# Optimization experiments

Measured on AMD Instinct MI355X. Metric: run time of the kernel, lower is better.

## Reference

```python
import jax, jax.numpy as jnp
import numpy as np

K = 3
TOP_K = 10
MASK_RATIO = 0.5
EPS_COS = 1e-8
EPS_DEG = 1e-6


def setup_inputs() -> dict:
    key = jax.random.key(0)
    ks = jax.random.split(key, 10)
    N, C, H, O, E = 4096, 128, 128, 64, 65536
    x = jax.random.normal(ks[0], (N, C), dtype=jnp.float32)
    edge_index = jax.random.randint(ks[1], (2, E), 0, N, dtype=jnp.int64)
    alpha = jnp.full((K,), 1.0 / K, dtype=jnp.float32)
    fusion_W = 0.02 * jax.random.normal(ks[2], (2 * H, H), dtype=jnp.float32)
    fusion_b = jnp.zeros((H,), dtype=jnp.float32)
    lin0_W = 0.02 * jax.random.normal(ks[3], (C, H), dtype=jnp.float32)
    lin0_b = jnp.zeros((H,), dtype=jnp.float32)
    lin1_W = 0.02 * jax.random.normal(ks[4], (H, O), dtype=jnp.float32)
    lin1_b = jnp.zeros((O,), dtype=jnp.float32)
    return {
        "x": x, "edge_index": edge_index, "alpha": alpha,
        "fusion_W": fusion_W, "fusion_b": fusion_b,
        "lin0_W": lin0_W, "lin0_b": lin0_b,
        "lin1_W": lin1_W, "lin1_b": lin1_b,
    }


def reference(x, edge_index, alpha, fusion_W, fusion_b, lin0_W, lin0_b, lin1_W, lin1_b):
    N = x.shape[0]
    # dense adjacency and its powers: A^0 = I (so A^0 @ x = x), A^1, A^2
    A = jnp.zeros((N, N), x.dtype).at[edge_index[0], edge_index[1]].set(1.0)
    A2 = A @ A
    hop_feats = jnp.stack([x, A @ x, A2 @ x], axis=0)  # [K, N, C]

    # per-node cosine-similarity top-k (self always included, cos=1)
    xn = x / (jnp.linalg.norm(x, axis=-1, keepdims=True) + EPS_COS)
    sim = xn @ xn.T  # [N, N]
    _, topk_idx = jax.lax.top_k(sim, TOP_K)  # [N, TOP_K]

    # random keep-mask per node, forced True at top-k neighbors
    mask = jax.random.uniform(jax.random.key(42), (N, N)) < MASK_RATIO
    rows = jnp.arange(N)[:, None]
    mask = mask.at[rows, topk_idx].set(True)
    Mf = mask.astype(x.dtype)  # [N, N]

    # alpha-weighted multi-hop aggregate, masked mean over selected nodes
    agg = jnp.einsum('k,knc->nc', alpha, hop_feats)  # [N, C]
    fused = (Mf @ agg) / (Mf.sum(axis=1, keepdims=True) + EPS_DEG)  # [N, C]

    h = jnp.concatenate([x, fused], axis=-1) @ fusion_W + fusion_b
    h = jax.nn.relu(h @ lin0_W + lin0_b)  # dropout inactive in eval
    out = h @ lin1_W + lin1_b
    return jax.nn.log_softmax(out, axis=1)
```

## Files before the change

### kernel.cpp

```cpp
#include <hip/hip_runtime.h>
#include <hip/hip_bf16.h>
#include <stdint.h>


#define N_NODES 4096
#define C_DIM   128
#define WPR     128
#define HALF_P  8388608u
#define TOPK    10
#define LSTR    13
#define JSPLIT  4

typedef __attribute__((ext_vector_type(8))) short bf16x8;
typedef __attribute__((ext_vector_type(4))) float f32x4;

__device__ __forceinline__ uint16_t f2bf(float f) {
    uint32_t u = __float_as_uint(f);
    return (uint16_t)((u + 0x7FFFu + ((u >> 16) & 1u)) >> 16);
}

__device__ __forceinline__ uint32_t rotl32(uint32_t v, int r) {
    return (v << r) | (v >> (32 - r));
}

__device__ __forceinline__ void threefry2x32(uint32_t k0, uint32_t k1,
                                             uint32_t x0, uint32_t x1,
                                             uint32_t& o0, uint32_t& o1) {
    uint32_t ks2 = k0 ^ k1 ^ 0x1BD11BDAu;
    x0 += k0; x1 += k1;
#define TF_ROUND(r) { x0 += x1; x1 = rotl32(x1, (r)); x1 ^= x0; }
    TF_ROUND(13) TF_ROUND(15) TF_ROUND(26) TF_ROUND(6)
    x0 += k1;  x1 += ks2 + 1u;
    TF_ROUND(17) TF_ROUND(29) TF_ROUND(16) TF_ROUND(24)
    x0 += ks2; x1 += k0 + 2u;
    TF_ROUND(13) TF_ROUND(15) TF_ROUND(26) TF_ROUND(6)
    x0 += k0;  x1 += k1 + 3u;
    TF_ROUND(17) TF_ROUND(29) TF_ROUND(16) TF_ROUND(24)
    x0 += k1;  x1 += ks2 + 4u;
    TF_ROUND(13) TF_ROUND(15) TF_ROUND(26) TF_ROUND(6)
    x0 += ks2; x1 += k0 + 5u;
#undef TF_ROUND
    o0 = x0; o1 = x1;
}

__global__ void scatter_kernel(const int* __restrict__ ei, int E,
                               uint32_t* __restrict__ Abits) {
    __shared__ int cnt_oddnz;
    int t = threadIdx.x;
    if (t == 0) cnt_oddnz = 0;
    __syncthreads();
    if (((const uint32_t*)ei)[2 * t + 1] != 0u) atomicAdd(&cnt_oddnz, 1);
    __syncthreads();
    bool is64 = (cnt_oddnz <= 8);
    int e = blockIdx.x * blockDim.x + t;
    if (e >= E) return;
    int src, dst;
    if (is64) { src = ei[2 * e]; dst = ei[2 * (E + e)]; }
    else      { src = ei[e];     dst = ei[E + e]; }
    src &= (N_NODES - 1);
    dst &= (N_NODES - 1);
    atomicOr(&Abits[src * WPR + (dst >> 5)], 1u << (dst & 31));
}

__global__ void spmm_kernel(const uint32_t* __restrict__ Abits,
                            const float* __restrict__ in,
                            float* __restrict__ out) {
    int i = blockIdx.x;
    int c = threadIdx.x;
    __shared__ uint32_t wbits[WPR];
    wbits[c] = Abits[i * WPR + c];
    __syncthreads();
    float acc = 0.f;
    for (int w = 0; w < WPR; ++w) {
        uint32_t bits = wbits[w];
        while (bits) {
            int b = __ffs(bits) - 1;
            bits &= bits - 1;
            acc += in[(w * 32 + b) * C_DIM + c];
        }
    }
    out[i * C_DIM + c] = acc;
}

__global__ void spmm2_agg_kernel(const uint32_t* __restrict__ Abits,
                                 const float* __restrict__ hop1,
                                 const float* __restrict__ xf,
                                 const float* __restrict__ alpha,
                                 float* __restrict__ agg) {
    int i = blockIdx.x;
    int c = threadIdx.x;
    __shared__ uint32_t wbits[WPR];
    wbits[c] = Abits[i * WPR + c];
    __syncthreads();
    float acc = 0.f;
    for (int w = 0; w < WPR; ++w) {
        uint32_t bits = wbits[w];
        while (bits) {
            int b = __ffs(bits) - 1;
            bits &= bits - 1;
            acc += hop1[(w * 32 + b) * C_DIM + c];
        }
    }
    agg[i * C_DIM + c] = alpha[0] * xf[i * C_DIM + c]
                       + alpha[1] * hop1[i * C_DIM + c]
                       + alpha[2] * acc;
}

__global__ void norm_kernel(const float* __restrict__ xf,
                            uint16_t* __restrict__ xnb) {
    int i = blockIdx.x;
    int c = threadIdx.x;
    float v = xf[i * C_DIM + c];
    float sq = v * v;
    #pragma unroll
    for (int off = 32; off >= 1; off >>= 1) sq += __shfl_xor(sq, off);
    __shared__ float ws[2];
    if ((c & 63) == 0) ws[c >> 6] = sq;
    __syncthreads();
    float tot = ws[0] + ws[1];
    xnb[i * C_DIM + c] = f2bf(v / (sqrtf(tot) + 1e-8f));
}

__global__ void transpose_bf_kernel(const float* __restrict__ agg,
                                    uint16_t* __restrict__ aggTb) {
    __shared__ float tile[32][33];
    int bi = blockIdx.x;
    int bc = blockIdx.y;
    int tx = threadIdx.x & 31, ty = threadIdx.x >> 5;
    #pragma unroll
    for (int r = 0; r < 32; r += 8)
        tile[ty + r][tx] = agg[(size_t)(bi * 32 + ty + r) * C_DIM + bc * 32 + tx];
    __syncthreads();
    #pragma unroll
    for (int r = 0; r < 32; r += 8)
        aggTb[(size_t)(bc * 32 + ty + r) * N_NODES + bi * 32 + tx] =
            f2bf(tile[tx][ty + r]);
}

__global__ void mask_kernel(uint32_t* __restrict__ Mbits,
                            int* __restrict__ degpre) {
    uint32_t tid = blockIdx.x * blockDim.x + threadIdx.x;
    uint32_t base = tid * 32u;
    uint32_t w0 = 0u, w1 = 0u;
    for (int k = 0; k < 32; ++k) {
        uint32_t o0, o1;
        threefry2x32(0u, 42u, base + k, HALF_P + base + k, o0, o1);
        w0 |= (uint32_t)((o0 >> 31) ^ 1u) << k;
        w1 |= (uint32_t)((o1 >> 31) ^ 1u) << k;
    }
    Mbits[tid] = w0;
    Mbits[(HALF_P >> 5) + tid] = w1;
    int p0 = __popc(w0), p1 = __popc(w1);
    #pragma unroll
    for (int off = 32; off >= 1; off >>= 1) {
        p0 += __shfl_xor(p0, off);
        p1 += __shfl_xor(p1, off);
    }
    if ((threadIdx.x & 63) == 0) {
        int row0 = (int)(tid >> 7);
        atomicAdd(&degpre[row0], p0);
        atomicAdd(&degpre[2048 + row0], p1);
    }
}

__launch_bounds__(512, 4)
__global__ void topk_kernel(const uint16_t* __restrict__ xnb,
                            float* __restrict__ topv,
                            int* __restrict__ topi) {
    int i0 = blockIdx.x * 16;
    int part = blockIdx.y;
    int t = threadIdx.x;
    int w = t >> 6;
    int lane = t & 63;
    int col = lane & 15;
    int quad = lane >> 4;

    __shared__ float    sval[32 * 16 * LSTR];
    __shared__ uint16_t sidx[32 * 16 * LSTR];

    bf16x8 bfi[4];
    #pragma unroll
    for (int s = 0; s < 4; ++s)
        bfi[s] = *(const bf16x8*)&xnb[(size_t)(i0 + col) * C_DIM + s * 32 + quad * 8];

    float tv[TOPK]; int ti[TOPK];
    #pragma unroll
    for (int k = 0; k < TOPK; ++k) { tv[k] = -1e30f; ti[k] = 0xFFFF; }

    int jt0 = part * 64 + w * 8;
    for (int p = 0; p < 8; ++p) {
        int j0 = (jt0 + p) * 16;
        f32x4 acc = {0.f, 0.f, 0.f, 0.f};
        #pragma unroll
        for (int s = 0; s < 4; ++s) {
            bf16x8 aj = *(const bf16x8*)&xnb[(size_t)(j0 + col) * C_DIM + s * 32 + quad * 8];
            acc = __builtin_amdgcn_mfma_f32_16x16x32_bf16(aj, bfi[s], acc, 0, 0, 0);
        }
        float m4 = fmaxf(fmaxf(acc[0], acc[1]), fmaxf(acc[2], acc[3]));
        if (m4 > tv[TOPK-1]) {
            #pragma unroll
            for (int r = 0; r < 4; ++r) {
                float d = acc[r];
                if (d > tv[TOPK-1]) {
                    int j = j0 + quad * 4 + r;
                    tv[TOPK-1] = d; ti[TOPK-1] = j;
                    #pragma unroll
                    for (int q = TOPK - 2; q >= 0; --q) {
                        if (tv[q+1] > tv[q]) {
                            float fv = tv[q]; tv[q] = tv[q+1]; tv[q+1] = fv;
                            int iv = ti[q];  ti[q] = ti[q+1];  ti[q+1] = iv;
                        }
                    }
                }
            }
        }
    }

    int base = ((w * 4 + quad) * 16 + col) * LSTR;
    #pragma unroll
    for (int k = 0; k < TOPK; ++k) {
        sval[base + k] = tv[k];
        sidx[base + k] = (uint16_t)ti[k];
    }

    int row = t & 15, L = t >> 4;
    for (int s = 16; s >= 1; s >>= 1) {
        __syncthreads();
        if (L < s) {
            int la = (L * 16 + row) * LSTR;
            int lb = ((L + s) * 16 + row) * LSTR;
            float ov[TOPK]; uint16_t oi[TOPK];
            int ia = 0, ib = 0;
            #pragma unroll
            for (int k = 0; k < TOPK; ++k) {
                float va = sval[la + ia], vb = sval[lb + ib];
                uint16_t xa = sidx[la + ia], xb = sidx[lb + ib];
                bool takeA = (va > vb) || (va == vb && xa < xb);
                if (takeA) { ov[k] = va; oi[k] = xa; ++ia; }
                else       { ov[k] = vb; oi[k] = xb; ++ib; }
            }
            #pragma unroll
            for (int k = 0; k < TOPK; ++k) { sval[la + k] = ov[k]; sidx[la + k] = oi[k]; }
        }
    }
    __syncthreads();
    if (t < 16) {
        size_t gi = (size_t)(part * N_NODES + i0 + t) * TOPK;
        #pragma unroll
        for (int k = 0; k < TOPK; ++k) {
            topv[gi + k] = sval[t * LSTR + k];
            topi[gi + k] = (int)sidx[t * LSTR + k];
        }
    }
}

__global__ void topmerge_kernel(const float* __restrict__ topv,
                                const int* __restrict__ topi,
                                const int* __restrict__ degpre,
                                uint32_t* __restrict__ Mbits,
                                float* __restrict__ deg) {
    int i = blockIdx.x * blockDim.x + threadIdx.x;
    if (i >= N_NODES) return;
    const float* v[JSPLIT]; const int* x[JSPLIT]; int ix[JSPLIT];
    #pragma unroll
    for (int q = 0; q < JSPLIT; ++q) {
        v[q] = topv + (size_t)(q * N_NODES + i) * TOPK;
        x[q] = topi + (size_t)(q * N_NODES + i) * TOPK;
        ix[q] = 0;
    }
    int newc = 0;
    #pragma unroll
    for (int k = 0; k < TOPK; ++k) {
        float bestv = -1e38f; int bestj = 0x7fffffff; int bestq = 0;
        #pragma unroll
        for (int q = 0; q < JSPLIT; ++q) {
            bool ok = ix[q] < TOPK;
            float fv = ok ? v[q][ix[q]] : -1e38f;
            int   jj = ok ? x[q][ix[q]] : 0x7fffffff;
            if (fv > bestv || (fv == bestv && jj < bestj)) {
                bestv = fv; bestj = jj; bestq = q;
            }
        }
        ++ix[bestq];
        uint32_t* wp = &Mbits[(size_t)i * WPR + (bestj >> 5)];
        uint32_t old = *wp, bit = 1u << (bestj & 31);
        newc += ((old & bit) == 0u);
        *wp = old | bit;
    }
    deg[i] = (float)(degpre[i] + newc);
}

__launch_bounds__(512, 2)
__global__ void fused_kernel(const uint32_t* __restrict__ Mbits,
                             const uint16_t* __restrict__ aggTb,
                             float* __restrict__ fpart) {
    int i0 = blockIdx.x * 16;
    int part = blockIdx.y;
    int t = threadIdx.x;
    int w = t >> 6;
    int lane = t & 63;
    int col = lane & 15;
    int quad = lane >> 4;

    const uint32_t* mrow = Mbits + (size_t)(i0 + col) * WPR;
    const uint16_t* brow = aggTb + (size_t)(w * 16 + col) * N_NODES;
    f32x4 acc[4];
    #pragma unroll
    for (int u = 0; u < 4; ++u) acc[u] = (f32x4){0.f, 0.f, 0.f, 0.f};

    int kbase = part * 2048;
    for (int k0 = kbase; k0 < kbase + 2048; k0 += 128) {
        uint4 mw4 = *(const uint4*)&mrow[k0 >> 5];
        uint32_t mws[4] = {mw4.x, mw4.y, mw4.z, mw4.w};
        #pragma unroll
        for (int u = 0; u < 4; ++u) {
            uint32_t byte = (mws[u] >> (quad * 8)) & 0xFFu;
            union { uint32_t uu[4]; bf16x8 v; } a;
            #pragma unroll
            for (int pp = 0; pp < 4; ++pp) {
                uint32_t lo = (byte >> (2 * pp)) & 1u;
                uint32_t hi = (byte >> (2 * pp + 1)) & 1u;
                a.uu[pp] = (lo ? 0x3F80u : 0u) | (hi ? 0x3F800000u : 0u);
            }
            bf16x8 b = *(const bf16x8*)&brow[k0 + u * 32 + quad * 8];
            acc[u] = __builtin_amdgcn_mfma_f32_16x16x32_bf16(a.v, b, acc[u], 0, 0, 0);
        }
    }
    #pragma unroll
    for (int r = 0; r < 4; ++r) {
        int il = quad * 4 + r;
        float s = (acc[0][r] + acc[1][r]) + (acc[2][r] + acc[3][r]);
        fpart[(size_t)part * (N_NODES * C_DIM)
              + (size_t)(i0 + il) * C_DIM + w * 16 + col] = s;
    }
}

__global__ void mlp_kernel(const float* __restrict__ xf,
                           const float* __restrict__ fpart,
                           const float* __restrict__ deg,
                           const float* __restrict__ fW, const float* __restrict__ fB,
                           const float* __restrict__ l0W, const float* __restrict__ l0B,
                           const float* __restrict__ l1W, const float* __restrict__ l1B,
                           float* __restrict__ out) {
    int i0 = blockIdx.x * 4;
    int t = threadIdx.x;
    __shared__ float lx[4][256];
    __shared__ float hb[4][128];
    const float* f0 = fpart;
    const float* f1 = fpart + (size_t)N_NODES * C_DIM;
    for (int r = t; r < 4 * 128; r += 128) {
        int row = r >> 7, c = r & 127;
        size_t idx = (size_t)(i0 + row) * C_DIM + c;
        lx[row][c] = xf[idx];
        lx[row][128 + c] = (f0[idx] + f1[idx]) / (deg[i0 + row] + 1e-6f);
    }
    __syncthreads();
    float acc[4];
    #pragma unroll
    for (int r = 0; r < 4; ++r) acc[r] = fB[t];
    for (int k = 0; k < 256; ++k) {
        float wv = fW[k * 128 + t];
        #pragma unroll
        for (int r = 0; r < 4; ++r) acc[r] = fmaf(lx[r][k], wv, acc[r]);
    }
    #pragma unroll
    for (int r = 0; r < 4; ++r) hb[r][t] = acc[r];
    __syncthreads();
    #pragma unroll
    for (int r = 0; r < 4; ++r) acc[r] = l0B[t];
    for (int k = 0; k < 128; ++k) {
        float wv = l0W[k * 128 + t];
        #pragma unroll
        for (int r = 0; r < 4; ++r) acc[r] = fmaf(hb[r][k], wv, acc[r]);
    }
    __syncthreads();
    #pragma unroll
    for (int r = 0; r < 4; ++r) lx[r][t] = fmaxf(acc[r], 0.f);
    __syncthreads();
    int o = t & 63, pr = t >> 6;
    #pragma unroll
    for (int rr = 0; rr < 2; ++rr) {
        int r = pr + 2 * rr;
        float a = l1B[o];
        for (int k = 0; k < 128; ++k)
            a = fmaf(lx[r][k], l1W[k * 64 + o], a);
        float m = a;
        #pragma unroll
        for (int off = 32; off >= 1; off >>= 1) m = fmaxf(m, __shfl_xor(m, off));
        float e = expf(a - m);
        float s = e;
        #pragma unroll
        for (int off = 32; off >= 1; off >>= 1) s += __shfl_xor(s, off);
        out[(size_t)(i0 + r) * 64 + o] = a - m - logf(s);
    }
}

extern "C" void kernel_launch(void* const* d_in, const int* in_sizes, int n_in,
                              void* d_out, int out_size, void* d_ws, size_t ws_size,
                              hipStream_t stream) {
    const float* xf    = (const float*)d_in[0];
    const int*   ei    = (const int*)d_in[1];
    const float* alpha = (const float*)d_in[2];
    const float* fW    = (const float*)d_in[3];
    const float* fB    = (const float*)d_in[4];
    const float* l0W   = (const float*)d_in[5];
    const float* l0B   = (const float*)d_in[6];
    const float* l1W   = (const float*)d_in[7];
    const float* l1B   = (const float*)d_in[8];
    float* out = (float*)d_out;
    const int E  = in_sizes[1] / 2;
    const int NC = N_NODES * C_DIM;

    char* p = (char*)d_ws;
    const size_t SZ = (size_t)NC * 4;
    uint32_t* Abits  = (uint32_t*)p; p += SZ;
    int*      degpre = (int*)p;      p += N_NODES * 4;
    float*    hop1   = (float*)p;    p += SZ;
    float*    agg    = (float*)p;    p += SZ;
    uint32_t* Mbits  = (uint32_t*)p; p += SZ;
    float*    fpart  = (float*)p;    p += 2 * SZ;
    uint16_t* xnb    = (uint16_t*)p; p += SZ / 2;
    uint16_t* aggTb  = (uint16_t*)p; p += SZ / 2;
    float*    deg    = (float*)p;    p += N_NODES * 4;
    float*    topv   = (float*)p;    p += (size_t)JSPLIT * N_NODES * TOPK * 4;
    int*      topi   = (int*)p;      p += (size_t)JSPLIT * N_NODES * TOPK * 4;

    hipMemsetAsync(Abits, 0, SZ + N_NODES * 4, stream);
    scatter_kernel<<<(E + 255) / 256, 256, 0, stream>>>(ei, E, Abits);
    spmm_kernel<<<N_NODES, 128, 0, stream>>>(Abits, xf, hop1);
    spmm2_agg_kernel<<<N_NODES, 128, 0, stream>>>(Abits, hop1, xf, alpha, agg);
    norm_kernel<<<N_NODES, 128, 0, stream>>>(xf, xnb);
    transpose_bf_kernel<<<dim3(128, 4), 256, 0, stream>>>(agg, aggTb);
    mask_kernel<<<(HALF_P >> 5) / 256, 256, 0, stream>>>(Mbits, degpre);
    topk_kernel<<<dim3(N_NODES / 16, JSPLIT), 512, 0, stream>>>(xnb, topv, topi);
    topmerge_kernel<<<N_NODES / 256, 256, 0, stream>>>(topv, topi, degpre, Mbits, deg);
    fused_kernel<<<dim3(N_NODES / 16, 2), 512, 0, stream>>>(Mbits, aggTb, fpart);
    mlp_kernel<<<N_NODES / 4, 128, 0, stream>>>(xf, fpart, deg,
                                                fW, fB, l0W, l0B, l1W, l1B, out);
}
```

Measured before the change: 250.7 us.

## Fuse norm, transpose, mask generation into spmm2; merge top-k into masked matmul

Folds the normalisation, bf16 transpose and threefry mask generation into the second SpMM kernel, so one launch produces agg, aggTb, xnb and the mask bits. The top-k merge moves into the masked-aggregation kernel, which now holds its mask slice in shared memory and ORs the top-k bits there rather than writing them back to global memory. The K dimension of that kernel is split four ways instead of two, with more blocks and higher launch-bounds occupancy, and the MLP kernel sums four partials. Together this cuts four launches and some global round trips. The cost is extra per-block serial merge work, repeated in all four split blocks, and the transposed aggTb store is now strided and uncoalesced.

```diff
diff --git a/kernel.cpp b/kernel.cpp
--- a/kernel.cpp
+++ b/kernel.cpp
@@ -82,14 +82,19 @@
     out[i * C_DIM + c] = acc;
 }
 
-__global__ void spmm2_agg_kernel(const uint32_t* __restrict__ Abits,
-                                 const float* __restrict__ hop1,
-                                 const float* __restrict__ xf,
-                                 const float* __restrict__ alpha,
-                                 float* __restrict__ agg) {
+__global__ void spmm2_combo_kernel(const uint32_t* __restrict__ Abits,
+                                   const float* __restrict__ hop1,
+                                   const float* __restrict__ xf,
+                                   const float* __restrict__ alpha,
+                                   float* __restrict__ agg,
+                                   uint16_t* __restrict__ aggTb,
+                                   uint16_t* __restrict__ xnb,
+                                   uint32_t* __restrict__ Mbits,
+                                   int* __restrict__ degpre) {
     int i = blockIdx.x;
     int c = threadIdx.x;
     __shared__ uint32_t wbits[WPR];
+    __shared__ float ws[2];
     wbits[c] = Abits[i * WPR + c];
     __syncthreads();
     float acc = 0.f;
@@ -101,63 +106,48 @@
             acc += hop1[(w * 32 + b) * C_DIM + c];
         }
     }
-    agg[i * C_DIM + c] = alpha[0] * xf[i * C_DIM + c]
-                       + alpha[1] * hop1[i * C_DIM + c]
-                       + alpha[2] * acc;
-}
-
-__global__ void norm_kernel(const float* __restrict__ xf,
-                            uint16_t* __restrict__ xnb) {
-    int i = blockIdx.x;
-    int c = threadIdx.x;
-    float v = xf[i * C_DIM + c];
-    float sq = v * v;
+    float xv  = xf[i * C_DIM + c];
+    float h1v = hop1[i * C_DIM + c];
+    float a = alpha[0] * xv + alpha[1] * h1v + alpha[2] * acc;
+    agg[i * C_DIM + c] = a;
+    aggTb[(size_t)c * N_NODES + i] = f2bf(a);
+
+    float sq = xv * xv;
     #pragma unroll
     for (int off = 32; off >= 1; off >>= 1) sq += __shfl_xor(sq, off);
-    __shared__ float ws[2];
     if ((c & 63) == 0) ws[c >> 6] = sq;
     __syncthreads();
     float tot = ws[0] + ws[1];
-    xnb[i * C_DIM + c] = f2bf(v / (sqrtf(tot) + 1e-8f));
-}
-
-__global__ void transpose_bf_kernel(const float* __restrict__ agg,
-                                    uint16_t* __restrict__ aggTb) {
-    __shared__ float tile[32][33];
-    int bi = blockIdx.x;
-    int bc = blockIdx.y;
-    int tx = threadIdx.x & 31, ty = threadIdx.x >> 5;
-    #pragma unroll
-    for (int r = 0; r < 32; r += 8)
-        tile[ty + r][tx] = agg[(size_t)(bi * 32 + ty + r) * C_DIM + bc * 32 + tx];
-    __syncthreads();
-    #pragma unroll
-    for (int r = 0; r < 32; r += 8)
-        aggTb[(size_t)(bc * 32 + ty + r) * N_NODES + bi * 32 + tx] =
-            f2bf(tile[tx][ty + r]);
-}
-
-__global__ void mask_kernel(uint32_t* __restrict__ Mbits,
-                            int* __restrict__ degpre) {
-    uint32_t tid = blockIdx.x * blockDim.x + threadIdx.x;
-    uint32_t base = tid * 32u;
+    xnb[i * C_DIM + c] = f2bf(xv / (sqrtf(tot) + 1e-8f));
+
+    uint32_t u = (uint32_t)(i * 128 + c);
+    uint32_t tid = u >> 1;
+    uint32_t halfb = u & 1u;
+    uint32_t base = tid * 32u + halfb * 16u;
     uint32_t w0 = 0u, w1 = 0u;
-    for (int k = 0; k < 32; ++k) {
+    for (int k = 0; k < 16; ++k) {
         uint32_t o0, o1;
         threefry2x32(0u, 42u, base + k, HALF_P + base + k, o0, o1);
         w0 |= (uint32_t)((o0 >> 31) ^ 1u) << k;
         w1 |= (uint32_t)((o1 >> 31) ^ 1u) << k;
     }
-    Mbits[tid] = w0;
-    Mbits[(HALF_P >> 5) + tid] = w1;
-    int p0 = __popc(w0), p1 = __popc(w1);
+    uint32_t w0o = (uint32_t)__shfl_xor((int)w0, 1);
+    uint32_t w1o = (uint32_t)__shfl_xor((int)w1, 1);
+    int p0 = 0, p1 = 0;
+    if (halfb == 0u) {
+        uint32_t W0 = w0 | (w0o << 16);
+        uint32_t W1 = w1 | (w1o << 16);
+        Mbits[tid] = W0;
+        Mbits[(HALF_P >> 5) + tid] = W1;
+        p0 = __popc(W0); p1 = __popc(W1);
+    }
     #pragma unroll
     for (int off = 32; off >= 1; off >>= 1) {
         p0 += __shfl_xor(p0, off);
         p1 += __shfl_xor(p1, off);
     }
-    if ((threadIdx.x & 63) == 0) {
-        int row0 = (int)(tid >> 7);
+    if ((c & 63) == 0) {
+        int row0 = i >> 1;
         atomicAdd(&degpre[row0], p0);
         atomicAdd(&degpre[2048 + row0], p1);
     }
@@ -254,46 +244,14 @@
     }
 }
 
-__global__ void topmerge_kernel(const float* __restrict__ topv,
-                                const int* __restrict__ topi,
-                                const int* __restrict__ degpre,
-                                uint32_t* __restrict__ Mbits,
-                                float* __restrict__ deg) {
-    int i = blockIdx.x * blockDim.x + threadIdx.x;
-    if (i >= N_NODES) return;
-    const float* v[JSPLIT]; const int* x[JSPLIT]; int ix[JSPLIT];
-    #pragma unroll
-    for (int q = 0; q < JSPLIT; ++q) {
-        v[q] = topv + (size_t)(q * N_NODES + i) * TOPK;
-        x[q] = topi + (size_t)(q * N_NODES + i) * TOPK;
-        ix[q] = 0;
-    }
-    int newc = 0;
-    #pragma unroll
-    for (int k = 0; k < TOPK; ++k) {
-        float bestv = -1e38f; int bestj = 0x7fffffff; int bestq = 0;
-        #pragma unroll
-        for (int q = 0; q < JSPLIT; ++q) {
-            bool ok = ix[q] < TOPK;
-            float fv = ok ? v[q][ix[q]] : -1e38f;
-            int   jj = ok ? x[q][ix[q]] : 0x7fffffff;
-            if (fv > bestv || (fv == bestv && jj < bestj)) {
-                bestv = fv; bestj = jj; bestq = q;
-            }
-        }
-        ++ix[bestq];
-        uint32_t* wp = &Mbits[(size_t)i * WPR + (bestj >> 5)];
-        uint32_t old = *wp, bit = 1u << (bestj & 31);
-        newc += ((old & bit) == 0u);
-        *wp = old | bit;
-    }
-    deg[i] = (float)(degpre[i] + newc);
-}
-
-__launch_bounds__(512, 2)
+__launch_bounds__(512, 4)
 __global__ void fused_kernel(const uint32_t* __restrict__ Mbits,
                              const uint16_t* __restrict__ aggTb,
-                             float* __restrict__ fpart) {
+                             const float* __restrict__ topv,
+                             const int* __restrict__ topi,
+                             const int* __restrict__ degpre,
+                             float* __restrict__ fpart,
+                             float* __restrict__ deg) {
     int i0 = blockIdx.x * 16;
     int part = blockIdx.y;
     int t = threadIdx.x;
@@ -302,19 +260,56 @@
     int col = lane & 15;
     int quad = lane >> 4;
 
-    const uint32_t* mrow = Mbits + (size_t)(i0 + col) * WPR;
+    __shared__ uint32_t smask[16][33];
+    smask[t >> 5][t & 31] =
+        Mbits[(size_t)(i0 + (t >> 5)) * WPR + part * 32 + (t & 31)];
+    __syncthreads();
+
+    if (t < 16) {
+        int i = i0 + t;
+        const float* v[JSPLIT]; const int* x[JSPLIT]; int ix[JSPLIT];
+        #pragma unroll
+        for (int q = 0; q < JSPLIT; ++q) {
+            v[q] = topv + (size_t)(q * N_NODES + i) * TOPK;
+            x[q] = topi + (size_t)(q * N_NODES + i) * TOPK;
+            ix[q] = 0;
+        }
+        int newc = 0;
+        int kw0 = part * 1024;
+        #pragma unroll
+        for (int k = 0; k < TOPK; ++k) {
+            float bestv = -1e38f; int bestj = 0x7fffffff; int bestq = 0;
+            #pragma unroll
+            for (int q = 0; q < JSPLIT; ++q) {
+                bool ok = ix[q] < TOPK;
+                float fv = ok ? v[q][ix[q]] : -1e38f;
+                int   jj = ok ? x[q][ix[q]] : 0x7fffffff;
+                if (fv > bestv || (fv == bestv && jj < bestj)) {
+                    bestv = fv; bestj = jj; bestq = q;
+                }
+            }
+            ++ix[bestq];
+            uint32_t mw = Mbits[(size_t)i * WPR + (bestj >> 5)];
+            newc += (int)(((mw >> (bestj & 31)) & 1u) == 0u);
+            int rel = bestj - kw0;
+            if (rel >= 0 && rel < 1024)
+                smask[t][rel >> 5] |= 1u << (bestj & 31);
+        }
+        if (part == 0) deg[i] = (float)(degpre[i] + newc);
+    }
+    __syncthreads();
+
     const uint16_t* brow = aggTb + (size_t)(w * 16 + col) * N_NODES;
+    int kbase = part * 1024;
     f32x4 acc[4];
     #pragma unroll
     for (int u = 0; u < 4; ++u) acc[u] = (f32x4){0.f, 0.f, 0.f, 0.f};
 
-    int kbase = part * 2048;
-    for (int k0 = kbase; k0 < kbase + 2048; k0 += 128) {
-        uint4 mw4 = *(const uint4*)&mrow[k0 >> 5];
-        uint32_t mws[4] = {mw4.x, mw4.y, mw4.z, mw4.w};
+    for (int k0 = 0; k0 < 1024; k0 += 128) {
         #pragma unroll
         for (int u = 0; u < 4; ++u) {
-            uint32_t byte = (mws[u] >> (quad * 8)) & 0xFFu;
+            uint32_t mw = smask[col][(k0 >> 5) + u];
+            uint32_t byte = (mw >> (quad * 8)) & 0xFFu;
             union { uint32_t uu[4]; bf16x8 v; } a;
             #pragma unroll
             for (int pp = 0; pp < 4; ++pp) {
@@ -322,7 +317,7 @@
                 uint32_t hi = (byte >> (2 * pp + 1)) & 1u;
                 a.uu[pp] = (lo ? 0x3F80u : 0u) | (hi ? 0x3F800000u : 0u);
             }
-            bf16x8 b = *(const bf16x8*)&brow[k0 + u * 32 + quad * 8];
+            bf16x8 b = *(const bf16x8*)&brow[kbase + k0 + u * 32 + quad * 8];
             acc[u] = __builtin_amdgcn_mfma_f32_16x16x32_bf16(a.v, b, acc[u], 0, 0, 0);
         }
     }
@@ -348,11 +343,14 @@
     __shared__ float hb[4][128];
     const float* f0 = fpart;
     const float* f1 = fpart + (size_t)N_NODES * C_DIM;
+    const float* f2 = fpart + (size_t)2 * N_NODES * C_DIM;
+    const float* f3 = fpart + (size_t)3 * N_NODES * C_DIM;
     for (int r = t; r < 4 * 128; r += 128) {
         int row = r >> 7, c = r & 127;
         size_t idx = (size_t)(i0 + row) * C_DIM + c;
         lx[row][c] = xf[idx];
-        lx[row][128 + c] = (f0[idx] + f1[idx]) / (deg[i0 + row] + 1e-6f);
+        lx[row][128 + c] = ((f0[idx] + f1[idx]) + (f2[idx] + f3[idx]))
+                           / (deg[i0 + row] + 1e-6f);
     }
     __syncthreads();
     float acc[4];
@@ -418,7 +416,7 @@
     float*    hop1   = (float*)p;    p += SZ;
     float*    agg    = (float*)p;    p += SZ;
     uint32_t* Mbits  = (uint32_t*)p; p += SZ;
-    float*    fpart  = (float*)p;    p += 2 * SZ;
+    float*    fpart  = (float*)p;    p += 4 * SZ;
     uint16_t* xnb    = (uint16_t*)p; p += SZ / 2;
     uint16_t* aggTb  = (uint16_t*)p; p += SZ / 2;
     float*    deg    = (float*)p;    p += N_NODES * 4;
@@ -428,13 +426,12 @@
     hipMemsetAsync(Abits, 0, SZ + N_NODES * 4, stream);
     scatter_kernel<<<(E + 255) / 256, 256, 0, stream>>>(ei, E, Abits);
     spmm_kernel<<<N_NODES, 128, 0, stream>>>(Abits, xf, hop1);
-    spmm2_agg_kernel<<<N_NODES, 128, 0, stream>>>(Abits, hop1, xf, alpha, agg);
-    norm_kernel<<<N_NODES, 128, 0, stream>>>(xf, xnb);
-    transpose_bf_kernel<<<dim3(128, 4), 256, 0, stream>>>(agg, aggTb);
-    mask_kernel<<<(HALF_P >> 5) / 256, 256, 0, stream>>>(Mbits, degpre);
+    spmm2_combo_kernel<<<N_NODES, 128, 0, stream>>>(Abits, hop1, xf, alpha,
+                                                    agg, aggTb, xnb, Mbits, degpre);
     topk_kernel<<<dim3(N_NODES / 16, JSPLIT), 512, 0, stream>>>(xnb, topv, topi);
-    topmerge_kernel<<<N_NODES / 256, 256, 0, stream>>>(topv, topi, degpre, Mbits, deg);
-    fused_kernel<<<dim3(N_NODES / 16, 2), 512, 0, stream>>>(Mbits, aggTb, fpart);
+    fused_kernel<<<dim3(N_NODES / 16, 4), 512, 0, stream>>>(Mbits, aggTb,
+                                                            topv, topi, degpre,
+                                                            fpart, deg);
     mlp_kernel<<<N_NODES / 4, 128, 0, stream>>>(xf, fpart, deg,
                                                 fW, fB, l0W, l0B, l1W, l1B, out);
 }
```

After: 245.1 us. 2.2% less time.
